# Performance work log

Hardware: AMD Instinct MI355X
Metric: run time of the kernel (lower is better)

Reference implementation:

```python
import jax, jax.numpy as jnp
import numpy as np

PSEUDO3D = True
DO_TUBE = True
DILATION_ITERATIONS = 1

# Neighbor offsets P2..P9 (clockwise from north), as in Zhang-Suen / skimage skeletonize
_OFFS = [(-1, 0), (-1, 1), (0, 1), (1, 1), (1, 0), (1, -1), (0, -1), (-1, -1)]


def _shift(a, dy, dx):
    # out[n, y, x] = a[n, y+dy, x+dx], zero-padded borders (same as skimage's 0-pad)
    N, H, W = a.shape
    p = jnp.pad(a, ((0, 0), (1, 1), (1, 1)))
    return p[:, 1 + dy:1 + dy + H, 1 + dx:1 + dx + W]


def _subiter(img, first):
    # One Zhang-Suen sub-iteration on a stack of 2D slices [N, H, W] (bool)
    P = [_shift(img, dy, dx) for dy, dx in _OFFS]
    B = sum(p.astype(jnp.int32) for p in P)            # nonzero-neighbor count
    seq = P + [P[0]]
    A = sum(((~seq[k]) & seq[k + 1]).astype(jnp.int32) for k in range(8))  # 0->1 transitions
    P2, P3, P4, P5, P6, P7, P8, P9 = P
    if first:
        c = (~(P2 & P4 & P6)) & (~(P4 & P6 & P8))
    else:
        c = (~(P2 & P4 & P8)) & (~(P2 & P6 & P8))
    remove = img & (B >= 2) & (B <= 6) & (A == 1) & c
    return img & ~remove


def _thin_stack(stack):
    # Zhang-Suen thinning of every 2D slice in a [N, H, W] bool stack, run to convergence.
    # All slices are processed in one while_loop; converged slices are fixed points, so
    # extra iterations are no-ops and the result matches per-slice skeletonize.
    def body(state):
        img, _ = state
        new = _subiter(_subiter(img, True), False)
        return new, jnp.any(new != img)

    def cond(state):
        return state[1]

    img, _ = jax.lax.while_loop(cond, body, (stack, jnp.array(True)))
    return img


def _dilate6(v):
    # scipy.ndimage.binary_dilation with the default 6-connected 3D structure, border 0
    D, H, W = v.shape
    p = jnp.pad(v, 1)
    out = v
    for dz, dy, dx in [(1, 0, 0), (-1, 0, 0), (0, 1, 0), (0, -1, 0), (0, 0, 1), (0, 0, -1)]:
        out = out | p[1 + dz:1 + dz + D, 1 + dy:1 + dy + H, 1 + dx:1 + dx + W]
    return out


def setup_inputs() -> dict:
    key = jax.random.key(0)
    gt = jax.random.randint(key, (1, 48, 384, 384), 0, 2).astype(jnp.float32)
    return {"gt_skel": gt}


def reference(gt_skel):
    vol = gt_skel[0]                      # squeeze(axis=0) -> [D, H, W]
    mask = vol == 1.0                     # bool
    skel = _thin_stack(mask)              # per z-slice skeletonize
    if PSEUDO3D:
        # per y-slice: mask[:, y, :] has shape [D, W]
        skel = skel | jnp.transpose(_thin_stack(jnp.transpose(mask, (1, 0, 2))), (1, 0, 2))
        # per x-slice: mask[:, :, x] has shape [D, H]
        skel = skel | jnp.transpose(_thin_stack(jnp.transpose(mask, (2, 0, 1))), (1, 2, 0))
    if DO_TUBE:
        for _ in range(DILATION_ITERATIONS):
            skel = _dilate6(skel)
    skel = skel & mask                    # skel &= gt_skel.astype(bool) (values are 0/1)
    return skel[None].astype(jnp.float32)
```

## Files before the change

kernel.cpp:

```cpp
#include <hip/hip_runtime.h>

typedef unsigned long long u64;

constexpr int D = 48, H = 384, W = 384;
constexpr int WPR = 6;
constexpr int PADW = 8;
constexpr int NVOX = D * H * W;
constexpr int NWVOL = D * H * WPR;
constexpr int MPAD2 = 52;
constexpr int NTILE = D * 36;

__device__ __forceinline__ void fa(u64 a, u64 b, u64 c, u64& s, u64& cy) {
  u64 x = a ^ b;
  s = x ^ c;
  cy = (a & b) | (c & x);
}

__device__ __forceinline__ u64 zs_regs(u64 w00, u64 w01, u64 w02,
                                       u64 w10, u64 w11, u64 w12,
                                       u64 w20, u64 w21, u64 w22, bool first) {
  const u64 P2 = w01;
  const u64 P3 = (w01 >> 1) | (w02 << 63);
  const u64 P4 = (w11 >> 1) | (w12 << 63);
  const u64 P5 = (w21 >> 1) | (w22 << 63);
  const u64 P6 = w21;
  const u64 P7 = (w21 << 1) | (w20 >> 63);
  const u64 P8 = (w11 << 1) | (w10 >> 63);
  const u64 P9 = (w01 << 1) | (w00 >> 63);

  u64 s1, c1, s2, c2, s3, c3, u0, u1, v1, v2;
  fa(P2, P3, P4, s1, c1);
  fa(P5, P6, P7, s2, c2);
  fa(P8, P9, 0ull, s3, c3);
  fa(s1, s2, s3, u0, u1);
  fa(c1, c2, c3, v1, v2);
  u64 b1 = u1 ^ v1, k2 = u1 & v1;
  u64 b2 = v2 ^ k2, b3 = v2 & k2;
  u64 condB = (b1 | b2 | b3) & ~(b3 | (b2 & b1 & u0));

  u64 t0 = ~P2 & P3, t1 = ~P3 & P4, t2 = ~P4 & P5, t3 = ~P5 & P6;
  u64 t4 = ~P6 & P7, t5 = ~P7 & P8, t6 = ~P8 & P9, t7 = ~P9 & P2;
  fa(t0, t1, t2, s1, c1);
  fa(t3, t4, t5, s2, c2);
  fa(t6, t7, 0ull, s3, c3);
  fa(s1, s2, s3, u0, u1);
  fa(c1, c2, c3, v1, v2);
  u64 a1 = u1 ^ v1, j2 = u1 & v1;
  u64 a2 = v2 ^ j2, a3 = v2 & j2;
  u64 condA = u0 & ~(a1 | a2 | a3);

  u64 cc = first ? ((~(P2 & P4 & P6)) & (~(P4 & P6 & P8)))
                 : ((~(P2 & P4 & P8)) & (~(P2 & P6 & P8)));
  return w11 & ~(condB & condA & cc);
}

__device__ __forceinline__ bool dirty3(const u64* U, int q) {
  const int pb = q + 64;
  const int w = pb >> 6, sh = pb & 63;
  u64 v = U[w] >> sh;
  if (sh > 61) v |= U[w + 1] << (64 - sh);
  return (v & 7ull) != 0;
}

template<int R, bool FIRST>
__device__ __forceinline__ void subpass(const u64* __restrict__ src, u64* __restrict__ dst,
                                        u64* rawW, const u64* rawPrev,
                                        u64* Uw, const u64* Ur,
                                        int* chgflag, int tid, int nthr) {
  constexpr int NP = (R + 2) * PADW;
  int anych = 0;
  for (int base = 0; base < NP; base += nthr) {
    const int idx = base + tid;
    int changed = 0;
    if (idx < NP) {
      const bool dirty = dirty3(Ur, idx - PADW - 1)
                       | dirty3(Ur, idx - 1)
                       | dirty3(Ur, idx + PADW - 1);
      if (dirty) {
        const u64 old = src[idx];
        u64 nw = 0;
        if (old) {
          nw = zs_regs(src[idx - PADW - 1], src[idx - PADW], src[idx - PADW + 1],
                       src[idx - 1], old, src[idx + 1],
                       src[idx + PADW - 1], src[idx + PADW], src[idx + PADW + 1], FIRST);
          changed = (nw != old);
        }
        dst[idx] = nw;
        anych |= changed;
      }
    }
    const u64 bal = __ballot(changed != 0);
    if ((tid & 63) == 0 && idx < NP) {
      const int mw = 1 + (idx >> 6);
      rawW[mw] = bal;
      Uw[mw] = bal | rawPrev[mw];
    }
  }
  if (anych) *chgflag = 1;
}

template<int R, int MODE>
__device__ __forceinline__ void thin_body(const u64* __restrict__ maskP,
                                          u64* __restrict__ dstBuf,
                                          int slice, u64* Abuf, u64* Bbuf,
                                          u64 (*raw)[MPAD2], u64 (*Um)[MPAD2],
                                          int* s_chg) {
  constexpr int NP = (R + 2) * PADW;
  constexpr int MW = (NP + 63) >> 6;
  const int tid = threadIdx.x;
  const int nthr = blockDim.x;

  if (MODE == 0 || MODE == 1) {
    for (int idx = tid; idx < NP; idx += nthr) {
      const int rp = idx >> 3, cp = idx & 7;
      u64 v = 0;
      if (rp >= 1 && rp <= R && cp >= 1 && cp <= 6) {
        if (MODE == 0) v = maskP[(slice * H + (rp - 1)) * WPR + (cp - 1)];
        else           v = maskP[((rp - 1) * H + slice) * WPR + (cp - 1)];
      }
      Abuf[idx] = v;
      Bbuf[idx] = 0;
    }
  } else {
    const int lane = tid & 63, wave = tid >> 6, nwv = nthr >> 6;
    const int xw = slice >> 6, xb = slice & 63;
    for (int w = wave; w < NP; w += nwv) {
      const int rp = w >> 3, cp = w & 7;
      u64 val = 0;
      if (rp >= 1 && rp <= R && cp >= 1 && cp <= 6) {
        const int c = (cp - 1) * 64 + lane;
        u64 bit = (maskP[((rp - 1) * H + c) * WPR + xw] >> xb) & 1ull;
        val = __ballot(bit != 0);
      }
      if (lane == 0) { Abuf[w] = val; Bbuf[w] = 0; }
    }
  }

  for (int t = tid; t < 4 * MPAD2; t += nthr) {
    const int arr = t / MPAD2, j = t - arr * MPAD2;
    const u64 v = ((arr & 1) && j >= 1 && j <= MW) ? ~0ull : 0ull;
    if (arr < 2) raw[arr][j] = v; else Um[arr - 2][j] = v;
  }
  if (tid < 2) s_chg[tid] = 0;
  __syncthreads();

  int k = 0;
  while (true) {
    subpass<R, true >(Abuf, Bbuf, raw[0], raw[1], Um[0], Um[1], &s_chg[k], tid, nthr);
    __syncthreads();
    if (tid == 0) s_chg[k ^ 1] = 0;
    subpass<R, false>(Bbuf, Abuf, raw[1], raw[0], Um[1], Um[0], &s_chg[k], tid, nthr);
    __syncthreads();
    if (s_chg[k] == 0) break;
    k ^= 1;
  }

  for (int idx = tid; idx < NP; idx += nthr) {
    const int rp = idx >> 3, cp = idx & 7;
    if (rp < 1 || rp > R || cp < 1 || cp > 6) continue;
    const u64 w = Abuf[idx];
    const int r = rp - 1, wc = cp - 1;
    if (MODE == 0)      dstBuf[(slice * H + r) * WPR + wc] = w;
    else if (MODE == 1) dstBuf[(r * H + slice) * WPR + wc] = w;
    else                dstBuf[(r * W + slice) * WPR + wc] = w;
  }
}

__global__ __launch_bounds__(1024) void thin_all(const u64* __restrict__ maskP,
                                                 u64* __restrict__ skelZ,
                                                 u64* __restrict__ skelY,
                                                 u64* __restrict__ skelX) {
  __shared__ u64 Abuf[(H + 2) * PADW];
  __shared__ u64 Bbuf[(H + 2) * PADW];
  __shared__ u64 raw[2][MPAD2];
  __shared__ u64 Um[2][MPAD2];
  __shared__ int s_chg[2];
  const int b = blockIdx.x;
  if (b < D) {
    thin_body<H, 0>(maskP, skelZ, b, Abuf, Bbuf, raw, Um, s_chg);
  } else if (b < D + H) {
    thin_body<D, 1>(maskP, skelY, b - D, Abuf, Bbuf, raw, Um, s_chg);
  } else {
    thin_body<D, 2>(maskP, skelX, b - D - H, Abuf, Bbuf, raw, Um, s_chg);
  }
}

__global__ void init_pack(const float* __restrict__ in, u64* __restrict__ maskP) {
  const int lane = threadIdx.x & 63;
  const int gwave = (blockIdx.x * blockDim.x + threadIdx.x) >> 6;
  const int nwaves = (gridDim.x * blockDim.x) >> 6;
  for (int widx = gwave; widx < NWVOL; widx += nwaves) {
    float v = in[(size_t)widx * 64 + lane];
    u64 w = __ballot(v == 1.0f);
    if (lane == 0) maskP[widx] = w;
  }
}

__global__ void transpose_x(const u64* __restrict__ skelX,
                            u64* __restrict__ skelXT) {
  const int gw = (blockIdx.x * blockDim.x + threadIdx.x) >> 6;
  const int lane = threadIdx.x & 63;
  const int z = gw / 36, rem = gw - z * 36;
  const int yw = rem / 6, xw = rem - yw * 6;
  const int x = xw * 64 + lane;
  const u64 wx = skelX[(z * W + x) * WPR + yw];
  u64 mine = 0;
  #pragma unroll 8
  for (int j = 0; j < 64; ++j) {
    u64 wj = __ballot((wx >> j) & 1ull);
    if (lane == j) mine = wj;
  }
  const int y = yw * 64 + lane;
  skelXT[(z * H + y) * WPR + xw] = mine;
}

__global__ __launch_bounds__(256) void dilate_expand(const u64* __restrict__ maskP,
                                                     const u64* __restrict__ sZ,
                                                     const u64* __restrict__ sY,
                                                     const u64* __restrict__ sXT,
                                                     float* __restrict__ out) {
  __shared__ u64 rw[64];
  const int tid = threadIdx.x;
  const int wbase = blockIdx.x * 64;
  if (tid < 64) {
    const int wi = wbase + tid;
    const int wc = wi % WPR;
    const int row = wi / WPR;
    const int y = row % H;
    const int z = row / H;
    const u64 S = sZ[wi] | sY[wi] | sXT[wi];
    const u64 L = (wc > 0) ? (sZ[wi - 1] | sY[wi - 1] | sXT[wi - 1]) : 0ull;
    const u64 Rw = (wc < WPR - 1) ? (sZ[wi + 1] | sY[wi + 1] | sXT[wi + 1]) : 0ull;
    u64 d = S | (S << 1) | (L >> 63) | (S >> 1) | (Rw << 63);
    if (y > 0)     d |= sZ[wi - WPR] | sY[wi - WPR] | sXT[wi - WPR];
    if (y < H - 1) d |= sZ[wi + WPR] | sY[wi + WPR] | sXT[wi + WPR];
    if (z > 0)     d |= sZ[wi - H * WPR] | sY[wi - H * WPR] | sXT[wi - H * WPR];
    if (z < D - 1) d |= sZ[wi + H * WPR] | sY[wi + H * WPR] | sXT[wi + H * WPR];
    rw[tid] = d & maskP[wi];
  }
  __syncthreads();
  float4* o4 = reinterpret_cast<float4*>(out + (size_t)wbase * 64);
  #pragma unroll
  for (int k = 0; k < 4; ++k) {
    const int f = tid + 256 * k;
    const u64 bits = rw[f >> 4] >> ((f & 15) * 4);
    float4 o;
    o.x = (float)(bits & 1ull);
    o.y = (float)((bits >> 1) & 1ull);
    o.z = (float)((bits >> 2) & 1ull);
    o.w = (float)((bits >> 3) & 1ull);
    o4[f] = o;
  }
}

extern "C" void kernel_launch(void* const* d_in, const int* in_sizes, int n_in,
                              void* d_out, int out_size, void* d_ws, size_t ws_size,
                              hipStream_t stream) {
  const float* in = (const float*)d_in[0];
  float* out = (float*)d_out;
  u64* wsw = (u64*)d_ws;
  u64* maskP = wsw;
  u64* skelZ = wsw + NWVOL;
  u64* skelY = wsw + 2 * NWVOL;
  u64* skelX = wsw + 3 * NWVOL;
  u64* skelXT = wsw + 4 * NWVOL;

  init_pack<<<1728, 256, 0, stream>>>(in, maskP);
  thin_all<<<D + H + W, 1024, 0, stream>>>(maskP, skelZ, skelY, skelX);
  transpose_x<<<(NTILE * 64) / 256, 256, 0, stream>>>(skelX, skelXT);
  dilate_expand<<<NWVOL / 64, 256, 0, stream>>>(maskP, skelZ, skelY, skelXT, out);
}
```

Baseline: 65.87 us.

## Use dense thinning for small Y/X slices and compute dirty masks per wave

Y and X slices are only 48 rows, so 50x8 padded words fit in one pass of 1024 threads. These slices now run a dense Zhang-Suen pass with no dirty-tracking bookkeeping or extra loops. For the large Z slices, the per-thread three-call dirty check is replaced by a per-wave computation that builds the dirty mask from four mask words with shifts and ORs. This cuts shared-memory reads and branching per pass, but the small slices now do full work every iteration even after most pixels have settled.

```diff
diff --git a/kernel.cpp b/kernel.cpp
--- a/kernel.cpp
+++ b/kernel.cpp
@@ -8,6 +8,7 @@
 constexpr int NVOX = D * H * W;
 constexpr int NWVOL = D * H * WPR;
 constexpr int MPAD2 = 52;
+constexpr int NXY = (D + 2) * PADW;
 constexpr int NTILE = D * 36;
 
 __device__ __forceinline__ void fa(u64 a, u64 b, u64 c, u64& s, u64& cy) {
@@ -54,12 +55,15 @@
   return w11 & ~(condB & condA & cc);
 }
 
-__device__ __forceinline__ bool dirty3(const u64* U, int q) {
-  const int pb = q + 64;
-  const int w = pb >> 6, sh = pb & 63;
-  u64 v = U[w] >> sh;
-  if (sh > 61) v |= U[w + 1] << (64 - sh);
-  return (v & 7ull) != 0;
+__device__ __forceinline__ u64 dirty_wave(const u64* __restrict__ U, int mw) {
+  const u64 A = U[mw - 1], B = U[mw], C = U[mw + 1], Dw = U[mw + 2];
+  const u64 smA = A | (A >> 1 | B << 63) | (A >> 2 | B << 62);
+  const u64 smB = B | (B >> 1 | C << 63) | (B >> 2 | C << 62);
+  const u64 smC = C | (C >> 1 | Dw << 63) | (C >> 2 | Dw << 62);
+  const u64 Dm9 = (smB << 9) | (smA >> 55);
+  const u64 Dm1 = (smB << 1) | (smA >> 63);
+  const u64 Dp7 = (smB >> 7) | (smC << 57);
+  return Dm9 | Dm1 | Dp7;
 }
 
 template<int R, bool FIRST>
@@ -73,10 +77,9 @@
     const int idx = base + tid;
     int changed = 0;
     if (idx < NP) {
-      const bool dirty = dirty3(Ur, idx - PADW - 1)
-                       | dirty3(Ur, idx - 1)
-                       | dirty3(Ur, idx + PADW - 1);
-      if (dirty) {
+      const int mw = 1 + (idx >> 6);
+      const u64 dmask = dirty_wave(Ur, mw);
+      if ((dmask >> (idx & 63)) & 1ull) {
         const u64 old = src[idx];
         u64 nw = 0;
         if (old) {
@@ -99,43 +102,43 @@
   if (anych) *chgflag = 1;
 }
 
-template<int R, int MODE>
-__device__ __forceinline__ void thin_body(const u64* __restrict__ maskP,
-                                          u64* __restrict__ dstBuf,
-                                          int slice, u64* Abuf, u64* Bbuf,
-                                          u64 (*raw)[MPAD2], u64 (*Um)[MPAD2],
-                                          int* s_chg) {
+template<bool FIRST>
+__device__ __forceinline__ void xy_dense(const u64* __restrict__ src, u64* __restrict__ dst,
+                                         int* chgflag, int tid) {
+  int anych = 0;
+  if (tid < NXY) {
+    const u64 old = src[tid];
+    u64 nw = 0;
+    if (old) {
+      nw = zs_regs(src[tid - PADW - 1], src[tid - PADW], src[tid - PADW + 1],
+                   src[tid - 1], old, src[tid + 1],
+                   src[tid + PADW - 1], src[tid + PADW], src[tid + PADW + 1], FIRST);
+      anych = (nw != old);
+    }
+    dst[tid] = nw;
+  }
+  if (anych) *chgflag = 1;
+}
+
+template<int R>
+__device__ __forceinline__ void thin_z(const u64* __restrict__ maskP,
+                                       u64* __restrict__ skelZ,
+                                       int slice, u64* Abuf, u64* Bbuf,
+                                       u64 (*raw)[MPAD2], u64 (*Um)[MPAD2],
+                                       int* s_chg) {
   constexpr int NP = (R + 2) * PADW;
   constexpr int MW = (NP + 63) >> 6;
   const int tid = threadIdx.x;
-  const int nthr = blockDim.x;
-
-  if (MODE == 0 || MODE == 1) {
-    for (int idx = tid; idx < NP; idx += nthr) {
-      const int rp = idx >> 3, cp = idx & 7;
-      u64 v = 0;
-      if (rp >= 1 && rp <= R && cp >= 1 && cp <= 6) {
-        if (MODE == 0) v = maskP[(slice * H + (rp - 1)) * WPR + (cp - 1)];
-        else           v = maskP[((rp - 1) * H + slice) * WPR + (cp - 1)];
-      }
-      Abuf[idx] = v;
-      Bbuf[idx] = 0;
-    }
-  } else {
-    const int lane = tid & 63, wave = tid >> 6, nwv = nthr >> 6;
-    const int xw = slice >> 6, xb = slice & 63;
-    for (int w = wave; w < NP; w += nwv) {
-      const int rp = w >> 3, cp = w & 7;
-      u64 val = 0;
-      if (rp >= 1 && rp <= R && cp >= 1 && cp <= 6) {
-        const int c = (cp - 1) * 64 + lane;
-        u64 bit = (maskP[((rp - 1) * H + c) * WPR + xw] >> xb) & 1ull;
-        val = __ballot(bit != 0);
-      }
-      if (lane == 0) { Abuf[w] = val; Bbuf[w] = 0; }
-    }
-  }
-
+  const int nthr = 1024;
+
+  for (int idx = tid; idx < NP; idx += nthr) {
+    const int rp = idx >> 3, cp = idx & 7;
+    u64 v = 0;
+    if (rp >= 1 && rp <= R && cp >= 1 && cp <= 6)
+      v = maskP[(slice * H + (rp - 1)) * WPR + (cp - 1)];
+    Abuf[idx] = v;
+    Bbuf[idx] = 0;
+  }
   for (int t = tid; t < 4 * MPAD2; t += nthr) {
     const int arr = t / MPAD2, j = t - arr * MPAD2;
     const u64 v = ((arr & 1) && j >= 1 && j <= MW) ? ~0ull : 0ull;
@@ -158,11 +161,61 @@
   for (int idx = tid; idx < NP; idx += nthr) {
     const int rp = idx >> 3, cp = idx & 7;
     if (rp < 1 || rp > R || cp < 1 || cp > 6) continue;
-    const u64 w = Abuf[idx];
-    const int r = rp - 1, wc = cp - 1;
-    if (MODE == 0)      dstBuf[(slice * H + r) * WPR + wc] = w;
-    else if (MODE == 1) dstBuf[(r * H + slice) * WPR + wc] = w;
-    else                dstBuf[(r * W + slice) * WPR + wc] = w;
+    skelZ[(slice * H + (rp - 1)) * WPR + (cp - 1)] = Abuf[idx];
+  }
+}
+
+template<int MODE>
+__device__ __forceinline__ void thin_xy(const u64* __restrict__ maskP,
+                                        u64* __restrict__ dstBuf,
+                                        int slice, u64* Abuf, u64* Bbuf,
+                                        int* s_chg) {
+  const int tid = threadIdx.x;
+
+  if (MODE == 1) {
+    if (tid < NXY) {
+      const int rp = tid >> 3, cp = tid & 7;
+      u64 v = 0;
+      if (rp >= 1 && rp <= D && cp >= 1 && cp <= 6)
+        v = maskP[((rp - 1) * H + slice) * WPR + (cp - 1)];
+      Abuf[tid] = v;
+      Bbuf[tid] = 0;
+    }
+  } else {
+    const int lane = tid & 63, wave = tid >> 6;
+    const int xw = slice >> 6, xb = slice & 63;
+    for (int w = wave; w < NXY; w += 16) {
+      const int rp = w >> 3, cp = w & 7;
+      u64 val = 0;
+      if (rp >= 1 && rp <= D && cp >= 1 && cp <= 6) {
+        const int c = (cp - 1) * 64 + lane;
+        u64 bit = (maskP[((rp - 1) * H + c) * WPR + xw] >> xb) & 1ull;
+        val = __ballot(bit != 0);
+      }
+      if (lane == 0) { Abuf[w] = val; Bbuf[w] = 0; }
+    }
+  }
+  if (tid < 2) s_chg[tid] = 0;
+  __syncthreads();
+
+  int k = 0;
+  while (true) {
+    xy_dense<true >(Abuf, Bbuf, &s_chg[k], tid);
+    __syncthreads();
+    if (tid == 0) s_chg[k ^ 1] = 0;
+    xy_dense<false>(Bbuf, Abuf, &s_chg[k], tid);
+    __syncthreads();
+    if (s_chg[k] == 0) break;
+    k ^= 1;
+  }
+
+  if (tid < NXY) {
+    const int rp = tid >> 3, cp = tid & 7;
+    if (rp >= 1 && rp <= D && cp >= 1 && cp <= 6) {
+      const u64 w = Abuf[tid];
+      if (MODE == 1) dstBuf[((rp - 1) * H + slice) * WPR + (cp - 1)] = w;
+      else           dstBuf[((rp - 1) * W + slice) * WPR + (cp - 1)] = w;
+    }
   }
 }
 
@@ -177,11 +230,11 @@
   __shared__ int s_chg[2];
   const int b = blockIdx.x;
   if (b < D) {
-    thin_body<H, 0>(maskP, skelZ, b, Abuf, Bbuf, raw, Um, s_chg);
+    thin_z<H>(maskP, skelZ, b, Abuf, Bbuf, raw, Um, s_chg);
   } else if (b < D + H) {
-    thin_body<D, 1>(maskP, skelY, b - D, Abuf, Bbuf, raw, Um, s_chg);
+    thin_xy<1>(maskP, skelY, b - D, Abuf, Bbuf, s_chg);
   } else {
-    thin_body<D, 2>(maskP, skelX, b - D - H, Abuf, Bbuf, raw, Um, s_chg);
+    thin_xy<2>(maskP, skelX, b - D - H, Abuf, Bbuf, s_chg);
   }
 }
 
```

New measurement: 61.97 us. -5.9%, faster.
